# Kernel optimization log

Hardware: AMD Instinct MI355X
Metric: run time of the kernel (lower is better)

Reference implementation:

```python
import jax, jax.numpy as jnp
import numpy as np
from jax import lax

N_NODES = 10000
N_EDGES = 320000


def setup_inputs() -> dict:
    key = jax.random.key(0)
    ks = jax.random.split(key, 11)
    s = 0.1  # weight init scale
    return {
        "x": jax.random.normal(ks[0], (N_NODES, 4), jnp.float32),
        "edge_index": jax.random.randint(ks[1], (2, N_EDGES), 0, N_NODES, dtype=jnp.int64),
        "edge_weight": jax.random.uniform(ks[2], (N_EDGES,), jnp.float32),
        "W1": s * jax.random.normal(ks[3], (120, 4, 64), jnp.float32),
        "b1": s * jax.random.normal(ks[4], (64,), jnp.float32),
        "W2": s * jax.random.normal(ks[5], (120, 64, 60), jnp.float32),
        "b2": s * jax.random.normal(ks[6], (60,), jnp.float32),
        "W3": s * jax.random.normal(ks[7], (20, 60, 30), jnp.float32),
        "b3": s * jax.random.normal(ks[8], (30,), jnp.float32),
        "W4": s * jax.random.normal(ks[9], (1, 30, 1), jnp.float32),
    }


def _propagate(h, src, dst, norm, n):
    # out[i] = sum_{e:(src_e -> i)} norm_e * h[src_e]   (PyG message+sum aggregate)
    return jax.ops.segment_sum(norm[:, None] * h[src], dst, num_segments=n)


def _cheb_conv(h, src, dst, norm, W, b, n):
    # PyG ChebConv: out = sum_k T_k(L_hat) h @ W_k (+ b), T_0=I, T_1=L_hat,
    # T_k = 2 L_hat T_{k-1} - T_{k-2}. W has shape [K, in, out].
    K = W.shape[0]
    out = h @ W[0]
    if K > 1:
        Tx1 = _propagate(h, src, dst, norm, n)
        out = out + Tx1 @ W[1]
        if K > 2:
            def step(carry, Wk):
                Tx0, Tx1, acc = carry
                Tx2 = 2.0 * _propagate(Tx1, src, dst, norm, n) - Tx0
                return (Tx1, Tx2, acc + Tx2 @ Wk), None
            (_, _, out), _ = lax.scan(step, (h, Tx1, out), W[2:])
    if b is not None:
        out = out + b
    return out


def reference(x, edge_index, edge_weight, W1, b1, W2, b2, W3, b3, W4):
    n = x.shape[0]
    src, dst = edge_index[0], edge_index[1]
    # Scaled Laplacian edge weights with lambda_max=2, sym norm, no self-loops:
    # L_hat = (2/lambda_max) * (I - D^{-1/2} A D^{-1/2}) - I = -D^{-1/2} A D^{-1/2}
    deg = jax.ops.segment_sum(edge_weight, src, num_segments=n)
    dis = jnp.where(deg > 0, deg ** -0.5, 0.0)
    norm = -dis[src] * edge_weight * dis[dst]
    h = jax.nn.silu(_cheb_conv(x, src, dst, norm, W1, b1, n))
    h = jax.nn.silu(_cheb_conv(h, src, dst, norm, W2, b2, n))
    h = jax.nn.silu(_cheb_conv(h, src, dst, norm, W3, b3, n))
    h = _cheb_conv(h, src, dst, norm, W4, None, n)
    return jax.nn.sigmoid(h)
```

## Files before the change

### kernel.cpp

```cpp
#include <hip/hip_runtime.h>
#include <math.h>

#define N_NODES 10000
#define N_EDGES 320000


__global__ void k_init(float* deg, int* cnt, int* fill, int n) {
    int i = blockIdx.x * blockDim.x + threadIdx.x;
    if (i < n) { deg[i] = 0.f; cnt[i] = 0; fill[i] = 0; }
}

__global__ void k_deg(const int* __restrict__ ei, const float* __restrict__ w,
                      float* deg, int E) {
    int e = blockIdx.x * blockDim.x + threadIdx.x;
    if (e < E) atomicAdd(&deg[ei[e]], w[e]);
}

__global__ void k_dis(float* deg, int n) {
    int i = blockIdx.x * blockDim.x + threadIdx.x;
    if (i < n) {
        float d = deg[i];
        deg[i] = (d > 0.f) ? (float)(1.0 / sqrt((double)d)) : 0.f;
    }
}

__global__ void k_norm(const int* __restrict__ ei, const float* __restrict__ w,
                       const float* __restrict__ dis, float* __restrict__ normw,
                       int* cnt, int E) {
    int e = blockIdx.x * blockDim.x + threadIdx.x;
    if (e < E) {
        int s = ei[e], d = ei[E + e];
        normw[e] = -dis[s] * w[e] * dis[d];
        atomicAdd(&cnt[d], 1);
    }
}

__global__ void k_scan(const int* __restrict__ cnt, int* __restrict__ rowptr, int n) {
    __shared__ int part[1024];
    const int PER = 10;
    int t = threadIdx.x;
    int base = t * PER;
    int local[PER];
    int s = 0;
    for (int j = 0; j < PER; j++) {
        int idx = base + j;
        int v = (idx < n) ? cnt[idx] : 0;
        local[j] = v; s += v;
    }
    part[t] = s;
    __syncthreads();
    for (int off = 1; off < 1024; off <<= 1) {
        int v = part[t];
        int u = (t >= off) ? part[t - off] : 0;
        __syncthreads();
        part[t] = v + u;
        __syncthreads();
    }
    int excl = (t > 0) ? part[t - 1] : 0;
    for (int j = 0; j < PER; j++) {
        int idx = base + j;
        if (idx < n) rowptr[idx] = excl;
        excl += local[j];
    }
    if (t == 1023) rowptr[n] = part[1023];
}

__global__ void k_fill(const int* __restrict__ ei, const float* __restrict__ normw,
                       const int* __restrict__ rowptr, int* fill,
                       int2* __restrict__ pr, int E) {
    int e = blockIdx.x * blockDim.x + threadIdx.x;
    if (e < E) {
        int d = ei[E + e];
        int pos = atomicAdd(&fill[d], 1);
        int idx = rowptr[d] + pos;
        pr[idx] = make_int2(ei[e] << 8, __float_as_int(normw[e]));
    }
}

__device__ __forceinline__ float gather_w(const char* __restrict__ tb,
                                          const int2* __restrict__ pr,
                                          int rb, int dg, int lane4) {
    float agg = 0.f;
    int e = 0;
    for (; e + 8 <= dg; e += 8) {
        int2 p[8]; float v[8];
#pragma unroll
        for (int u = 0; u < 8; u++) p[u] = pr[rb + e + u];
#pragma unroll
        for (int u = 0; u < 8; u++)
            v[u] = *(const float*)(tb + (unsigned)p[u].x + lane4);
#pragma unroll
        for (int u = 0; u < 8; u++)
            agg = fmaf(__int_as_float(p[u].y), v[u], agg);
    }
    if (e < dg) {
        int2 p[8]; float v[8];
#pragma unroll
        for (int u = 0; u < 8; u++) p[u] = pr[(e + u < dg) ? (rb + e + u) : rb];
#pragma unroll
        for (int u = 0; u < 8; u++)
            v[u] = *(const float*)(tb + (unsigned)p[u].x + lane4);
#pragma unroll
        for (int u = 0; u < 8; u++) {
            float w = (e + u < dg) ? __int_as_float(p[u].y) : 0.f;
            agg = fmaf(w, v[u], agg);
        }
    }
    return agg;
}

__device__ __forceinline__ float gather_n(const char* __restrict__ tb,
                                          const int2* __restrict__ pr,
                                          int rb, int dg, int lc4, int eo) {
    float agg = 0.f;
    int e = eo;
    for (; e + 32 <= dg; e += 32) {
        int2 p0 = pr[rb + e];
        int2 p1 = pr[rb + e + 16];
        float v0 = *(const float*)(tb + ((unsigned)p0.x >> 4) + lc4);
        float v1 = *(const float*)(tb + ((unsigned)p1.x >> 4) + lc4);
        agg = fmaf(__int_as_float(p0.y), v0, agg);
        agg = fmaf(__int_as_float(p1.y), v1, agg);
    }
    for (; e < dg; e += 16) {
        int2 p = pr[rb + e];
        agg = fmaf(__int_as_float(p.y),
                   *(const float*)(tb + ((unsigned)p.x >> 4) + lc4), agg);
    }
    agg += __shfl_xor(agg, 4);
    agg += __shfl_xor(agg, 8);
    agg += __shfl_xor(agg, 16);
    agg += __shfl_xor(agg, 32);
    return agg;
}

template <int CI, int CO>
__device__ __forceinline__ void dense(float& acc, float t2v,
                                      const float* __restrict__ Wk, int lane) {
#pragma unroll
    for (int c = 0; c < CI; c++) {
        float tb = __int_as_float(__builtin_amdgcn_readlane(__float_as_int(t2v), c));
        float wv;
        if (CO < 64) wv = (lane < CO) ? Wk[c * CO + lane] : 0.f;
        else         wv = Wk[c * CO + lane];
        acc = fmaf(tb, wv, acc);
    }
}


template <int CI, int CO, int MODE, int LAST>
__global__ __launch_bounds__(256) void k_wide(
    const int* __restrict__ rowptr, const int2* __restrict__ pr,
    const float* __restrict__ hin,
    const float* __restrict__ t0, const float* __restrict__ t1,
    float* __restrict__ t2, float* __restrict__ accb,
    const float* __restrict__ Wk, const float* __restrict__ bias,
    const float* __restrict__ W4, float* __restrict__ outp)
{
    int tid = threadIdx.x;
    int lane = tid & 63;
    int node = blockIdx.x * 4 + (tid >> 6);
    int rb = rowptr[node];
    int dg = rowptr[node + 1] - rb;
    int lane4 = lane * 4;

    float acc, t2v;
    if (MODE == 1) {
        float hr = hin[node * 64 + lane];
        acc = (lane < CO) ? bias[lane] : 0.f;
        dense<CI, CO>(acc, hr, Wk, lane);
        t2v = gather_w((const char*)hin, pr, rb, dg, lane4);
        dense<CI, CO>(acc, t2v, Wk + CI * CO, lane);
    } else {
        acc = accb[node * 64 + lane];
        float t0r = t0[node * 64 + lane];
        float agg = gather_w((const char*)t1, pr, rb, dg, lane4);
        t2v = fmaf(2.f, agg, -t0r);
        dense<CI, CO>(acc, t2v, Wk, lane);
    }

    if (LAST == 0) {
        accb[node * 64 + lane] = acc;
        t2[node * 64 + lane] = t2v;
    } else if (LAST == 1) {
        outp[node * 64 + lane] = acc / (1.f + expf(-acc));
    } else {
        float h = acc / (1.f + expf(-acc));
        float w4 = (lane < 30) ? W4[lane] : 0.f;
        float p = h * w4;
        p += __shfl_xor(p, 1);
        p += __shfl_xor(p, 2);
        p += __shfl_xor(p, 4);
        p += __shfl_xor(p, 8);
        p += __shfl_xor(p, 16);
        p += __shfl_xor(p, 32);
        if (lane == 0) outp[node] = 1.f / (1.f + expf(-p));
    }
}

template <int MODE, int LAST>
__global__ __launch_bounds__(256) void k_narrow(
    const int* __restrict__ rowptr, const int2* __restrict__ pr,
    const float* __restrict__ xin,
    const float* __restrict__ t0, const float* __restrict__ t1,
    float* __restrict__ t2, float* __restrict__ accb,
    const float* __restrict__ Wk, const float* __restrict__ bias,
    float* __restrict__ outp)
{
    int tid = threadIdx.x;
    int lane = tid & 63;
    int node = blockIdx.x * 4 + (tid >> 6);
    int rb = rowptr[node];
    int dg = rowptr[node + 1] - rb;
    int lc = lane & 3, eo = lane >> 2, lc4 = lc * 4;

    float acc, t2v;
    if (MODE == 1) {
        float xr = xin[node * 4 + lc];
        acc = bias[lane];
        dense<4, 64>(acc, xr, Wk, lane);
        t2v = gather_n((const char*)xin, pr, rb, dg, lc4, eo);
        dense<4, 64>(acc, t2v, Wk + 4 * 64, lane);
    } else {
        acc = accb[node * 64 + lane];
        float t0r = t0[node * 4 + lc];
        float agg = gather_n((const char*)t1, pr, rb, dg, lc4, eo);
        t2v = fmaf(2.f, agg, -t0r);
        dense<4, 64>(acc, t2v, Wk, lane);
    }

    if (LAST == 0) {
        accb[node * 64 + lane] = acc;
        if (lane < 4) t2[node * 4 + lane] = t2v;
    } else {
        outp[node * 64 + lane] = acc / (1.f + expf(-acc));
    }
}


extern "C" void kernel_launch(void* const* d_in, const int* in_sizes, int n_in,
                              void* d_out, int out_size, void* d_ws, size_t ws_size,
                              hipStream_t stream) {
    const float* x  = (const float*)d_in[0];
    const int*   ei = (const int*)d_in[1];
    const float* ew = (const float*)d_in[2];
    const float* W1 = (const float*)d_in[3];
    const float* b1 = (const float*)d_in[4];
    const float* W2 = (const float*)d_in[5];
    const float* b2 = (const float*)d_in[6];
    const float* W3 = (const float*)d_in[7];
    const float* b3 = (const float*)d_in[8];
    const float* W4 = (const float*)d_in[9];
    float* out = (float*)d_out;

    const int n = N_NODES, E = N_EDGES;

    char* ws = (char*)d_ws;
    size_t off = 0;
    auto alloc = [&](size_t bytes) -> void* {
        void* p = ws + off;
        off += (bytes + 255) & ~(size_t)255;
        return p;
    };
    float* deg    = (float*)alloc(n * 4);
    int*   cnt    = (int*)alloc(n * 4);
    int*   fill   = (int*)alloc(n * 4);
    int*   rowptr = (int*)alloc((n + 4) * 4);
    float* normw  = (float*)alloc((size_t)E * 4);
    int2*  pr     = (int2*)alloc((size_t)E * 8);
    float* t4a  = (float*)alloc(n * 4 * 4);
    float* t4b  = (float*)alloc(n * 4 * 4);
    float* t4c  = (float*)alloc(n * 4 * 4);
    float* tba  = (float*)alloc(n * 64 * 4);
    float* tbb  = (float*)alloc(n * 64 * 4);
    float* tbc  = (float*)alloc(n * 64 * 4);
    float* accb = (float*)alloc(n * 64 * 4);
    float* h1   = (float*)alloc(n * 64 * 4);
    float* h2   = (float*)alloc(n * 64 * 4);
    (void)ws_size; (void)n_in; (void)in_sizes; (void)out_size;

    k_init<<<(n + 255) / 256, 256, 0, stream>>>(deg, cnt, fill, n);
    k_deg <<<(E + 255) / 256, 256, 0, stream>>>(ei, ew, deg, E);
    k_dis <<<(n + 255) / 256, 256, 0, stream>>>(deg, n);
    k_norm<<<(E + 255) / 256, 256, 0, stream>>>(ei, ew, deg, normw, cnt, E);
    k_scan<<<1, 1024, 0, stream>>>(cnt, rowptr, n);
    k_fill<<<(E + 255) / 256, 256, 0, stream>>>(ei, normw, rowptr, fill, pr, E);

    const int G = n / 4;

    {
        const int K = 120;
        float* tb[3] = {t4a, t4b, t4c};
        k_narrow<1, 0><<<G, 256, 0, stream>>>(rowptr, pr, x, nullptr, nullptr,
                                              tb[1], accb, W1, b1, nullptr);
        for (int k = 2; k < K; k++) {
            const float* t0p = (k == 2) ? x : tb[(k - 2) % 3];
            const float* t1p = tb[(k - 1) % 3];
            const float* Wk = W1 + (size_t)k * 4 * 64;
            if (k < K - 1)
                k_narrow<2, 0><<<G, 256, 0, stream>>>(rowptr, pr, nullptr, t0p, t1p,
                                                      tb[k % 3], accb, Wk, nullptr, nullptr);
            else
                k_narrow<2, 1><<<G, 256, 0, stream>>>(rowptr, pr, nullptr, t0p, t1p,
                                                      nullptr, accb, Wk, nullptr, h1);
        }
    }

    {
        const int K = 120;
        float* tb[3] = {tba, tbb, tbc};
        k_wide<64, 60, 1, 0><<<G, 256, 0, stream>>>(rowptr, pr, h1, nullptr, nullptr,
                                                    tb[1], accb, W2, b2, nullptr, nullptr);
        for (int k = 2; k < K; k++) {
            const float* t0p = (k == 2) ? h1 : tb[(k - 2) % 3];
            const float* t1p = tb[(k - 1) % 3];
            const float* Wk = W2 + (size_t)k * 64 * 60;
            if (k < K - 1)
                k_wide<64, 60, 2, 0><<<G, 256, 0, stream>>>(rowptr, pr, nullptr, t0p, t1p,
                                                            tb[k % 3], accb, Wk, nullptr,
                                                            nullptr, nullptr);
            else
                k_wide<64, 60, 2, 1><<<G, 256, 0, stream>>>(rowptr, pr, nullptr, t0p, t1p,
                                                            nullptr, accb, Wk, nullptr,
                                                            nullptr, h2);
        }
    }

    {
        const int K = 20;
        float* tb[3] = {tba, tbb, tbc};
        k_wide<60, 30, 1, 0><<<G, 256, 0, stream>>>(rowptr, pr, h2, nullptr, nullptr,
                                                    tb[1], accb, W3, b3, nullptr, nullptr);
        for (int k = 2; k < K; k++) {
            const float* t0p = (k == 2) ? h2 : tb[(k - 2) % 3];
            const float* t1p = tb[(k - 1) % 3];
            const float* Wk = W3 + (size_t)k * 60 * 30;
            if (k < K - 1)
                k_wide<60, 30, 2, 0><<<G, 256, 0, stream>>>(rowptr, pr, nullptr, t0p, t1p,
                                                            tb[k % 3], accb, Wk, nullptr,
                                                            nullptr, nullptr);
            else
                k_wide<60, 30, 2, 2><<<G, 256, 0, stream>>>(rowptr, pr, nullptr, t0p, t1p,
                                                            nullptr, accb, Wk, nullptr,
                                                            W4, out);
        }
    }
}
```

Measured before the change: 3.419 ms.

## Fuse layer-1 Chebyshev recurrence into one persistent kernel with grid barriers

Replaces the 119 per-order layer-1 kernel launches with a single persistent kernel of 250 blocks, each owning 40 nodes. Each block caches its CSR edge slice in LDS, keeps the T_{k-1}/T_{k-2} terms and accumulators in registers, and separates Chebyshev orders with a software grid barrier. This removes launch overhead and the per-step accumulator round-trips through global memory for the narrow layer. The cost is a spin barrier per order, which relies on all 250 blocks being co-resident, plus relaxed atomic stores to publish T_k.

```diff
diff --git a/kernel.cpp b/kernel.cpp
--- a/kernel.cpp
+++ b/kernel.cpp
@@ -3,11 +3,40 @@
 
 #define N_NODES 10000
 #define N_EDGES 320000
-
-
-__global__ void k_init(float* deg, int* cnt, int* fill, int n) {
+#define GRID 250
+#define BLOCK 512
+#define NPW 5
+#define NPB 40
+#define ECAP 2048
+
+__device__ __forceinline__ void ast(float* p, float v) {
+    __hip_atomic_store(p, v, __ATOMIC_RELAXED, __HIP_MEMORY_SCOPE_AGENT);
+}
+
+__device__ __forceinline__ void gbar(int* bar) {
+    __builtin_amdgcn_fence(__ATOMIC_RELEASE, "workgroup");
+    __syncthreads();
+    if (threadIdx.x == 0) {
+        int* ctr = bar;
+        int* gen = bar + 64;
+        int g = __hip_atomic_load(gen, __ATOMIC_RELAXED, __HIP_MEMORY_SCOPE_AGENT);
+        int a = __hip_atomic_fetch_add(ctr, 1, __ATOMIC_RELEASE, __HIP_MEMORY_SCOPE_AGENT);
+        if (a == GRID - 1) {
+            __hip_atomic_store(ctr, 0, __ATOMIC_RELAXED, __HIP_MEMORY_SCOPE_AGENT);
+            __hip_atomic_store(gen, g + 1, __ATOMIC_RELEASE, __HIP_MEMORY_SCOPE_AGENT);
+        } else {
+            while (__hip_atomic_load(gen, __ATOMIC_RELAXED, __HIP_MEMORY_SCOPE_AGENT) == g)
+                __builtin_amdgcn_s_sleep(1);
+        }
+        __builtin_amdgcn_fence(__ATOMIC_ACQUIRE, "agent");
+    }
+    __syncthreads();
+}
+
+__global__ void k_init(float* deg, int* cnt, int* fill, int* bar, int n) {
     int i = blockIdx.x * blockDim.x + threadIdx.x;
     if (i < n) { deg[i] = 0.f; cnt[i] = 0; fill[i] = 0; }
+    if (i < 128) bar[i] = 0;
 }
 
 __global__ void k_deg(const int* __restrict__ ei, const float* __restrict__ w,
@@ -77,6 +106,33 @@
     }
 }
 
+template <bool L>
+__device__ __forceinline__ float gather_n(const char* __restrict__ tb,
+                                          const int2* ls_pr,
+                                          const int2* __restrict__ g_pr,
+                                          int rb, int dg, int lc4, int eo) {
+    float agg = 0.f;
+    int e = eo;
+    for (; e + 32 <= dg; e += 32) {
+        int2 p0 = L ? ls_pr[rb + e]      : g_pr[rb + e];
+        int2 p1 = L ? ls_pr[rb + e + 16] : g_pr[rb + e + 16];
+        float v0 = *(const float*)(tb + ((unsigned)p0.x >> 4) + lc4);
+        float v1 = *(const float*)(tb + ((unsigned)p1.x >> 4) + lc4);
+        agg = fmaf(__int_as_float(p0.y), v0, agg);
+        agg = fmaf(__int_as_float(p1.y), v1, agg);
+    }
+    for (; e < dg; e += 16) {
+        int2 p = L ? ls_pr[rb + e] : g_pr[rb + e];
+        agg = fmaf(__int_as_float(p.y),
+                   *(const float*)(tb + ((unsigned)p.x >> 4) + lc4), agg);
+    }
+    agg += __shfl_xor(agg, 4);
+    agg += __shfl_xor(agg, 8);
+    agg += __shfl_xor(agg, 16);
+    agg += __shfl_xor(agg, 32);
+    return agg;
+}
+
 __device__ __forceinline__ float gather_w(const char* __restrict__ tb,
                                           const int2* __restrict__ pr,
                                           int rb, int dg, int lane4) {
@@ -109,29 +165,21 @@
     return agg;
 }
 
-__device__ __forceinline__ float gather_n(const char* __restrict__ tb,
-                                          const int2* __restrict__ pr,
-                                          int rb, int dg, int lc4, int eo) {
-    float agg = 0.f;
-    int e = eo;
-    for (; e + 32 <= dg; e += 32) {
-        int2 p0 = pr[rb + e];
-        int2 p1 = pr[rb + e + 16];
-        float v0 = *(const float*)(tb + ((unsigned)p0.x >> 4) + lc4);
-        float v1 = *(const float*)(tb + ((unsigned)p1.x >> 4) + lc4);
-        agg = fmaf(__int_as_float(p0.y), v0, agg);
-        agg = fmaf(__int_as_float(p1.y), v1, agg);
-    }
-    for (; e < dg; e += 16) {
-        int2 p = pr[rb + e];
-        agg = fmaf(__int_as_float(p.y),
-                   *(const float*)(tb + ((unsigned)p.x >> 4) + lc4), agg);
-    }
-    agg += __shfl_xor(agg, 4);
-    agg += __shfl_xor(agg, 8);
-    agg += __shfl_xor(agg, 16);
-    agg += __shfl_xor(agg, 32);
-    return agg;
+template <int CI, int CO>
+__device__ __forceinline__ void dense_step(float (&acc)[NPW], const float (&t2v)[NPW],
+                                           const float* lsW, int lane)
+{
+#pragma unroll
+    for (int c = 0; c < CI; c++) {
+        float wv = lsW[c * CO + lane];
+#pragma unroll
+        for (int j = 0; j < NPW; j++)
+            acc[j] = fmaf(__shfl(t2v[j], c), wv, acc[j]);
+    }
+}
+
+__device__ __forceinline__ void stage_w(const float* __restrict__ Wg, float* lsW, int cnt) {
+    for (int i = threadIdx.x; i < cnt; i += BLOCK) lsW[i] = Wg[i];
 }
 
 template <int CI, int CO>
@@ -147,6 +195,87 @@
     }
 }
 
+__global__ __launch_bounds__(BLOCK, 2) void layer1_persistent(
+    const float* __restrict__ x,
+    const int* __restrict__ rowptr, const int2* __restrict__ g_pr,
+    const float* __restrict__ W1, const float* __restrict__ b1,
+    float* t4a, float* t4b, float* __restrict__ h1, int* bar)
+{
+    __shared__ int2  ls_pr[ECAP];
+    __shared__ float lsW[4 * 64];
+
+    const int K = 120, CI = 4, CO = 64;
+    int tid = threadIdx.x;
+    int w = tid >> 6, lane = tid & 63;
+
+    int nb0 = blockIdx.x * NPB;
+    int eb = rowptr[nb0];
+    int ee = rowptr[nb0 + NPB];
+    int ecnt = ee - eb;
+    bool use_lds = (ecnt <= ECAP);
+    if (use_lds) {
+        for (int i = tid; i < ecnt; i += BLOCK) ls_pr[i] = g_pr[eb + i];
+    }
+
+    int nodes[NPW], rbj[NPW], dgj[NPW];
+    int node0 = nb0 + w * NPW;
+#pragma unroll
+    for (int j = 0; j < NPW; j++) {
+        nodes[j] = node0 + j;
+        int r0 = rowptr[nodes[j]], r1 = rowptr[nodes[j] + 1];
+        dgj[j] = r1 - r0;
+        rbj[j] = use_lds ? (r0 - eb) : r0;
+    }
+    __syncthreads();
+
+    float t1r[NPW], t0r[NPW], acc[NPW];
+#pragma unroll
+    for (int j = 0; j < NPW; j++) t1r[j] = x[nodes[j] * 4 + (lane & 3)];
+
+    stage_w(W1, lsW, CI * CO);
+    float bv = b1[lane];
+    __syncthreads();
+#pragma unroll
+    for (int j = 0; j < NPW; j++) { acc[j] = bv; t0r[j] = t1r[j]; }
+    dense_step<CI, CO>(acc, t1r, lsW, lane);
+
+    float* tb[2] = {t4a, t4b};
+    int cur = 1;
+    int eo = lane >> 2, lc4 = (lane & 3) * 4;
+
+#pragma unroll 1
+    for (int k = 1; k < K; k++) {
+        __syncthreads();
+        stage_w(W1 + k * CI * CO, lsW, CI * CO);
+        const char* gs = (const char*)((k == 1) ? x : tb[cur]);
+        float t2v[NPW];
+#pragma unroll
+        for (int j = 0; j < NPW; j++) {
+            float agg = use_lds
+                ? gather_n<true >(gs, ls_pr, g_pr, rbj[j], dgj[j], lc4, eo)
+                : gather_n<false>(gs, ls_pr, g_pr, rbj[j], dgj[j], lc4, eo);
+            t2v[j] = (k == 1) ? agg : fmaf(2.f, agg, -t0r[j]);
+        }
+        __syncthreads();
+        dense_step<CI, CO>(acc, t2v, lsW, lane);
+#pragma unroll
+        for (int j = 0; j < NPW; j++) { t0r[j] = t1r[j]; t1r[j] = t2v[j]; }
+        if (k < K - 1) {
+            float* gd = tb[cur ^ 1];
+#pragma unroll
+            for (int j = 0; j < NPW; j++)
+                if (lane < 4) ast(&gd[nodes[j] * 4 + lane], t2v[j]);
+            cur ^= 1;
+            gbar(bar);
+        }
+    }
+
+#pragma unroll
+    for (int j = 0; j < NPW; j++) {
+        float a = acc[j];
+        h1[nodes[j] * 64 + lane] = a / (1.f + expf(-a));
+    }
+}
 
 template <int CI, int CO, int MODE, int LAST>
 __global__ __launch_bounds__(256) void k_wide(
@@ -198,46 +327,6 @@
     }
 }
 
-template <int MODE, int LAST>
-__global__ __launch_bounds__(256) void k_narrow(
-    const int* __restrict__ rowptr, const int2* __restrict__ pr,
-    const float* __restrict__ xin,
-    const float* __restrict__ t0, const float* __restrict__ t1,
-    float* __restrict__ t2, float* __restrict__ accb,
-    const float* __restrict__ Wk, const float* __restrict__ bias,
-    float* __restrict__ outp)
-{
-    int tid = threadIdx.x;
-    int lane = tid & 63;
-    int node = blockIdx.x * 4 + (tid >> 6);
-    int rb = rowptr[node];
-    int dg = rowptr[node + 1] - rb;
-    int lc = lane & 3, eo = lane >> 2, lc4 = lc * 4;
-
-    float acc, t2v;
-    if (MODE == 1) {
-        float xr = xin[node * 4 + lc];
-        acc = bias[lane];
-        dense<4, 64>(acc, xr, Wk, lane);
-        t2v = gather_n((const char*)xin, pr, rb, dg, lc4, eo);
-        dense<4, 64>(acc, t2v, Wk + 4 * 64, lane);
-    } else {
-        acc = accb[node * 64 + lane];
-        float t0r = t0[node * 4 + lc];
-        float agg = gather_n((const char*)t1, pr, rb, dg, lc4, eo);
-        t2v = fmaf(2.f, agg, -t0r);
-        dense<4, 64>(acc, t2v, Wk, lane);
-    }
-
-    if (LAST == 0) {
-        accb[node * 64 + lane] = acc;
-        if (lane < 4) t2[node * 4 + lane] = t2v;
-    } else {
-        outp[node * 64 + lane] = acc / (1.f + expf(-acc));
-    }
-}
-
-
 extern "C" void kernel_launch(void* const* d_in, const int* in_sizes, int n_in,
                               void* d_out, int out_size, void* d_ws, size_t ws_size,
                               hipStream_t stream) {
@@ -268,9 +357,9 @@
     int*   rowptr = (int*)alloc((n + 4) * 4);
     float* normw  = (float*)alloc((size_t)E * 4);
     int2*  pr     = (int2*)alloc((size_t)E * 8);
+    int*   bar    = (int*)alloc(128 * 4);
     float* t4a  = (float*)alloc(n * 4 * 4);
     float* t4b  = (float*)alloc(n * 4 * 4);
-    float* t4c  = (float*)alloc(n * 4 * 4);
     float* tba  = (float*)alloc(n * 64 * 4);
     float* tbb  = (float*)alloc(n * 64 * 4);
     float* tbc  = (float*)alloc(n * 64 * 4);
@@ -279,32 +368,17 @@
     float* h2   = (float*)alloc(n * 64 * 4);
     (void)ws_size; (void)n_in; (void)in_sizes; (void)out_size;
 
-    k_init<<<(n + 255) / 256, 256, 0, stream>>>(deg, cnt, fill, n);
+    k_init<<<(n + 255) / 256, 256, 0, stream>>>(deg, cnt, fill, bar, n);
     k_deg <<<(E + 255) / 256, 256, 0, stream>>>(ei, ew, deg, E);
     k_dis <<<(n + 255) / 256, 256, 0, stream>>>(deg, n);
     k_norm<<<(E + 255) / 256, 256, 0, stream>>>(ei, ew, deg, normw, cnt, E);
     k_scan<<<1, 1024, 0, stream>>>(cnt, rowptr, n);
     k_fill<<<(E + 255) / 256, 256, 0, stream>>>(ei, normw, rowptr, fill, pr, E);
 
+    layer1_persistent<<<GRID, BLOCK, 0, stream>>>(x, rowptr, pr, W1, b1,
+                                                  t4a, t4b, h1, bar);
+
     const int G = n / 4;
-
-    {
-        const int K = 120;
-        float* tb[3] = {t4a, t4b, t4c};
-        k_narrow<1, 0><<<G, 256, 0, stream>>>(rowptr, pr, x, nullptr, nullptr,
-                                              tb[1], accb, W1, b1, nullptr);
-        for (int k = 2; k < K; k++) {
-            const float* t0p = (k == 2) ? x : tb[(k - 2) % 3];
-            const float* t1p = tb[(k - 1) % 3];
-            const float* Wk = W1 + (size_t)k * 4 * 64;
-            if (k < K - 1)
-                k_narrow<2, 0><<<G, 256, 0, stream>>>(rowptr, pr, nullptr, t0p, t1p,
-                                                      tb[k % 3], accb, Wk, nullptr, nullptr);
-            else
-                k_narrow<2, 1><<<G, 256, 0, stream>>>(rowptr, pr, nullptr, t0p, t1p,
-                                                      nullptr, accb, Wk, nullptr, h1);
-        }
-    }
 
     {
         const int K = 120;
```

New measurement: 4.122 ms. 1.21x slower.
